# Kernel tuning notes

Measured on AMD Instinct MI355X. Metric: run time of the kernel, lower is better.

Reference implementation:

```python
import jax, jax.numpy as jnp
import numpy as np

WH, WW = 12, 12          # window height/width
N = WH * WW              # tokens per window (144)
HEADS = 16
DIM = 1024
C = DIM // 2             # attention channel dim (512)
HEAD_DIM = C // HEADS    # 32


def _rel_pos_index(wh, ww):
    ch, cw = np.arange(wh), np.arange(ww)
    coords = np.stack(np.meshgrid(ch, cw, indexing='ij')).reshape(2, -1)  # [2, N]
    rel = (coords[:, :, None] - coords[:, None, :]).transpose(1, 2, 0)    # [N, N, 2]
    rel = rel.copy()
    rel[:, :, 0] += wh - 1
    rel[:, :, 1] += ww - 1
    rel[:, :, 0] *= 2 * ww - 1
    return rel.sum(-1)  # [N, N] int


def _layernorm(x, g, b, eps=1e-5):
    mu = jnp.mean(x, axis=-1, keepdims=True)
    var = jnp.mean(jnp.square(x - mu), axis=-1, keepdims=True)
    return (x - mu) * jax.lax.rsqrt(var + eps) * g + b


def setup_inputs():
    key = jax.random.key(0)
    ks = jax.random.split(key, 10)
    std = 0.02
    inp = {
        'x': jax.random.normal(ks[0], (256, N, DIM), jnp.float32),
        'template': jax.random.normal(ks[1], (64, N, DIM), jnp.float32),
        'mask0': jnp.zeros((16, N, N), jnp.float32),
        'mask1': jnp.zeros((4, N, N), jnp.float32),
        's_H': 48, 's_W': 48, 't_H': 24, 't_W': 24,
        'rpb_table': jax.random.normal(ks[2], ((2 * WH - 1) * (2 * WW - 1), HEADS), jnp.float32) * std,
        'w_ps': jax.random.normal(ks[3], (DIM, C), jnp.float32) * std,
        'b_ps': jnp.zeros((C,), jnp.float32),
        'g_ps': jnp.ones((C,), jnp.float32),
        'be_ps': jnp.zeros((C,), jnp.float32),
        'w_pt': jax.random.normal(ks[4], (DIM, C), jnp.float32) * std,
        'b_pt': jnp.zeros((C,), jnp.float32),
        'g_pt': jnp.ones((C,), jnp.float32),
        'be_pt': jnp.zeros((C,), jnp.float32),
        'w_qkv': jax.random.normal(ks[5], (C, 3 * C), jnp.float32) * std,
        'b_qkv': jnp.zeros((3 * C,), jnp.float32),
        'w_tr': jax.random.normal(ks[6], (C, DIM), jnp.float32) * std,
        'b_tr': jnp.zeros((DIM,), jnp.float32),
        'w_sr': jax.random.normal(ks[7], (C, DIM), jnp.float32) * std,
        'b_sr': jnp.zeros((DIM,), jnp.float32),
    }
    return inp


def reference(x, template, mask0, mask1, s_H, s_W, t_H, t_W,
              rpb_table, w_ps, b_ps, g_ps, be_ps, w_pt, b_pt, g_pt, be_pt,
              w_qkv, b_qkv, w_tr, b_tr, w_sr, b_sr):
    scale = HEAD_DIM ** (-0.5)
    search_attn = _layernorm(x @ w_ps + b_ps, g_ps, be_ps)          # [Sw, N, C]
    template_attn = _layernorm(template @ w_pt + b_pt, g_pt, be_pt)  # [Tw, N, C]
    Sw, Tw = search_attn.shape[0], template_attn.shape[0]
    xa = jnp.concatenate([template_attn, search_attn], axis=0)      # [B_, N, C]
    B_, n, c = xa.shape

    qkv = (xa @ w_qkv + b_qkv).reshape(B_, n, 3, HEADS, HEAD_DIM)
    q = qkv[:, :, 0].transpose(0, 2, 1, 3) * scale  # [B_, H, N, Dh]
    k = qkv[:, :, 1].transpose(0, 2, 1, 3)
    v = qkv[:, :, 2].transpose(0, 2, 1, 3)

    idx = _rel_pos_index(WH, WW)  # numpy constant [N, N]
    bias = rpb_table[idx.reshape(-1)].reshape(n, n, HEADS).transpose(2, 0, 1)  # [H, N, N]

    attn = jnp.einsum('bhnd,bhmd->bhnm', q, k) + bias[None]  # [B_, H, N, N]

    attn_t, attn_s = attn[:Tw], attn[Tw:]
    nWs = mask0.shape[0]
    attn_s = (attn_s.reshape(Sw // nWs, nWs, HEADS, n, n) + mask0[None, :, None]).reshape(Sw, HEADS, n, n)
    nWt = mask1.shape[0]
    attn_t = (attn_t.reshape(Tw // nWt, nWt, HEADS, n, n) + mask1[None, :, None]).reshape(Tw, HEADS, n, n)
    attn = jax.nn.softmax(jnp.concatenate([attn_t, attn_s], axis=0), axis=-1)

    out = jnp.einsum('bhnm,bhmd->bhnd', attn, v).transpose(0, 2, 1, 3).reshape(B_, n, c)
    template_out = out[:Tw] @ w_tr + b_tr  # [Tw, N, DIM]
    search_out = out[Tw:] @ w_sr + b_sr    # [Sw, N, DIM]
    return (template_out, search_out)
```

## Files before the change

kernel.cpp:

```cpp
#include <hip/hip_runtime.h>


using s16x8 = __attribute__((ext_vector_type(8))) short;
using f32x4 = __attribute__((ext_vector_type(4))) float;
typedef __attribute__((ext_vector_type(2))) unsigned u32x2;

#define NTOK 144
#define NHEADS 16
#define CDIM 512
#define TROWS 9216
#define SROWS 36864
#define TOTROWS 46080
#define NWIN 320
#define NCLS 20

__device__ __forceinline__ unsigned short f2bf(float f) {
  unsigned u = __float_as_uint(f);
  u += 0x7fffu + ((u >> 16) & 1u);
  return (unsigned short)(u >> 16);
}
__device__ __forceinline__ float bf2f(unsigned short u) {
  return __uint_as_float(((unsigned)u) << 16);
}
__device__ __forceinline__ s16x8 mk8(unsigned a, unsigned b, unsigned c, unsigned d) {
  union { unsigned u[4]; s16x8 v; } x;
  x.u[0] = a; x.u[1] = b; x.u[2] = c; x.u[3] = d;
  return x.v;
}

__device__ __forceinline__ void gld16(const unsigned short* g, short* l) {
  __builtin_amdgcn_global_load_lds(
      (const __attribute__((address_space(1))) unsigned int*)g,
      (__attribute__((address_space(3))) unsigned int*)l, 16, 0, 0);
}


__global__ void transpose_cast(const float* __restrict__ w,
                               unsigned short* __restrict__ wT, int Kd, int Nd) {
  int i = blockIdx.x * 256 + threadIdx.x;
  if (i >= Kd * Nd) return;
  int n = i / Kd, k = i % Kd;
  wT[i] = f2bf(w[(size_t)k * Nd + n]);
}

__global__ __launch_bounds__(256) void cast_bf16(const float* __restrict__ in,
                                                 unsigned short* __restrict__ out, int n8) {
  int i = blockIdx.x * 256 + threadIdx.x;
  if (i >= n8) return;
  const float4* p = (const float4*)in + (size_t)i * 2;
  float4 f0 = p[0], f1 = p[1];
  s16x8 o;
  o[0] = (short)f2bf(f0.x); o[1] = (short)f2bf(f0.y);
  o[2] = (short)f2bf(f0.z); o[3] = (short)f2bf(f0.w);
  o[4] = (short)f2bf(f1.x); o[5] = (short)f2bf(f1.y);
  o[6] = (short)f2bf(f1.z); o[7] = (short)f2bf(f1.w);
  *(s16x8*)&out[(size_t)i * 8] = o;
}

__global__ void build_cmb(const float* __restrict__ rpb, const float* __restrict__ m0,
                          const float* __restrict__ m1, unsigned short* __restrict__ cmb) {
  int i = blockIdx.x * 256 + threadIdx.x;
  if (i >= NCLS * NHEADS * NTOK * NTOK) return;
  int cls = i / (NHEADS * NTOK * NTOK);
  int rem = i % (NHEADS * NTOK * NTOK);
  int h = rem / (NTOK * NTOK);
  int ij = rem % (NTOK * NTOK);
  int qi = ij / NTOK, kj = ij % NTOK;
  int dh = qi / 12 - kj / 12 + 11;
  int dw = qi % 12 - kj % 12 + 11;
  float bias = rpb[(dh * 23 + dw) * NHEADS + h];
  float mv = (cls < 4) ? m1[(size_t)cls * NTOK * NTOK + ij]
                       : m0[(size_t)(cls - 4) * NTOK * NTOK + ij];
  cmb[i] = f2bf(bias + mv);
}

template<int EPI>
__global__ __launch_bounds__(256) void gemm_glds(
    const unsigned short* __restrict__ Ab,
    const unsigned short* __restrict__ BTt, const unsigned short* __restrict__ BTs,
    const float* __restrict__ biast, const float* __restrict__ biass,
    void* __restrict__ Cout, int M, int N, int K)
{
  __shared__ short As[128 * 64];
  __shared__ short Bs[128 * 64];
  const int t = threadIdx.x;
  const int lane = t & 63, wv = t >> 6, lg = lane >> 4, lc = lane & 15;
  const int bn = blockIdx.x * 128, bm = blockIdx.y * 128;
  const bool isT = bm < TROWS;
  const unsigned short* BT = isT ? BTt : BTs;
  const float* bias = isT ? biast : biass;

  const int srow = 32 * wv + (lane >> 3);
  const int scol = (((lane & 7) ^ ((lane >> 3) & 7))) * 8;
  const unsigned short* aSrc = Ab + (size_t)(bm + srow) * K + scol;
  const unsigned short* bSrc = BT + (size_t)(bn + srow) * K + scol;
  const size_t rowK8 = (size_t)8 * K;

  f32x4 acc[2][8] = {};

  for (int kt = 0; kt < K; kt += 64) {
    __syncthreads();
#pragma unroll
    for (int i = 0; i < 4; i++) {
      gld16(aSrc + kt + i * rowK8, &As[(wv * 4 + i) * 512]);
      gld16(bSrc + kt + i * rowK8, &Bs[(wv * 4 + i) * 512]);
    }
    __syncthreads();
#pragma unroll
    for (int kk = 0; kk < 2; kk++) {
      const int csw = 8 * ((4 * kk + lg) ^ (lc & 7));
      const int r0 = wv * 32 + lc, r1 = r0 + 16;
      s16x8 a0 = *(const s16x8*)&As[r0 * 64 + csw];
      s16x8 a1 = *(const s16x8*)&As[r1 * 64 + csw];
#pragma unroll
      for (int nt = 0; nt < 8; nt++) {
        s16x8 bfr = *(const s16x8*)&Bs[(nt * 16 + lc) * 64 + csw];
        acc[0][nt] = __builtin_amdgcn_mfma_f32_16x16x32_bf16(a0, bfr, acc[0][nt], 0, 0, 0);
        acc[1][nt] = __builtin_amdgcn_mfma_f32_16x16x32_bf16(a1, bfr, acc[1][nt], 0, 0, 0);
      }
    }
  }

#pragma unroll
  for (int mt = 0; mt < 2; mt++) {
    const int rbase = bm + wv * 32 + mt * 16 + lg * 4;
#pragma unroll
    for (int nt = 0; nt < 8; nt++) {
      const int cg = bn + nt * 16 + lc;
#pragma unroll
      for (int r = 0; r < 4; r++) {
        const int rg = rbase + r;
        float val = acc[mt][nt][r] + bias[cg];
        if (EPI == 2) {
          ((float*)Cout)[(size_t)rg * N + cg] = val;
        } else {
          if (EPI == 1 && cg < 512) val *= 0.17677669529663687f;
          ((unsigned short*)Cout)[(size_t)rg * N + cg] = f2bf(val);
        }
      }
    }
  }
}

__global__ __launch_bounds__(256) void ln_kernel(
    unsigned short* __restrict__ xa,
    const float* __restrict__ g_pt, const float* __restrict__ be_pt,
    const float* __restrict__ g_ps, const float* __restrict__ be_ps)
{
  const int row = blockIdx.x * 4 + (threadIdx.x >> 6);
  const int lane = threadIdx.x & 63;
  const bool isT = row < TROWS;
  const float* gg = isT ? g_pt : g_ps;
  const float* be = isT ? be_pt : be_ps;
  unsigned short* p = xa + (size_t)row * CDIM;
  const int c0 = lane * 8;

  s16x8 v8 = *(const s16x8*)&p[c0];
  float f[8];
  float s = 0.f, s2 = 0.f;
#pragma unroll
  for (int i = 0; i < 8; i++) {
    float xv = bf2f((unsigned short)v8[i]);
    f[i] = xv; s += xv; s2 += xv * xv;
  }
#pragma unroll
  for (int d = 1; d < 64; d <<= 1) { s += __shfl_xor(s, d); s2 += __shfl_xor(s2, d); }
  float mu = s * (1.f / CDIM);
  float var = s2 * (1.f / CDIM) - mu * mu;
  float rs = rsqrtf(var + 1e-5f);

  float4 g0 = *(const float4*)&gg[c0], g1 = *(const float4*)&gg[c0 + 4];
  float4 e0 = *(const float4*)&be[c0], e1 = *(const float4*)&be[c0 + 4];
  float gv[8] = {g0.x, g0.y, g0.z, g0.w, g1.x, g1.y, g1.z, g1.w};
  float ev[8] = {e0.x, e0.y, e0.z, e0.w, e1.x, e1.y, e1.z, e1.w};
  s16x8 o;
#pragma unroll
  for (int i = 0; i < 8; i++)
    o[i] = (short)f2bf((f[i] - mu) * rs * gv[i] + ev[i]);
  *(s16x8*)&p[c0] = o;
}

__global__ __launch_bounds__(576) void attn_kernel(
    const unsigned short* __restrict__ qkv, const unsigned short* __restrict__ cmb,
    unsigned short* __restrict__ outp)
{
  __shared__ short VT[32 * 168];
  const int w = blockIdx.x >> 4, h = blockIdx.x & 15;
  const int t = threadIdx.x;
  const unsigned short* qb = qkv + (size_t)w * NTOK * 1536;
  const int hq = h * 32;

  {
    const int n = t >> 2, d0 = (t & 3) * 8;
    s16x8 vv = *(const s16x8*)&qb[(size_t)n * 1536 + 1024 + hq + d0];
#pragma unroll
    for (int i = 0; i < 8; i++) VT[(d0 + i) * 168 + n] = vv[i];
  }
  if (t < 512) VT[(t >> 4) * 168 + 144 + (t & 15)] = 0;
  __syncthreads();

  const int lane = t & 63, wv = t >> 6, lg = lane >> 4, lc = lane & 15;
  const int q = wv * 16 + lc;
  const f32x4 zero = {0.f, 0.f, 0.f, 0.f};

  const s16x8 qf = *(const s16x8*)&qb[(size_t)q * 1536 + hq + lg * 8];

  const int cls = (w < 64) ? (w & 3) : 4 + ((w - 64) & 15);
  const unsigned short* cm =
      cmb + ((size_t)cls * NHEADS + h) * (NTOK * NTOK) + (size_t)q * NTOK;
  uint2 cmr[9];
#pragma unroll
  for (int nt = 0; nt < 9; nt++)
    cmr[nt] = *(const uint2*)&cm[nt * 16 + lg * 4];

  f32x4 accS[9];
#pragma unroll
  for (int nt = 0; nt < 9; nt++) {
    s16x8 kf = *(const s16x8*)&qb[(size_t)(nt * 16 + lc) * 1536 + 512 + hq + lg * 8];
    accS[nt] = __builtin_amdgcn_mfma_f32_16x16x32_bf16(kf, qf, zero, 0, 0, 0);
  }

  float mx = -1e30f;
#pragma unroll
  for (int nt = 0; nt < 9; nt++) {
    accS[nt][0] += bf2f((unsigned short)(cmr[nt].x & 0xffff));
    accS[nt][1] += bf2f((unsigned short)(cmr[nt].x >> 16));
    accS[nt][2] += bf2f((unsigned short)(cmr[nt].y & 0xffff));
    accS[nt][3] += bf2f((unsigned short)(cmr[nt].y >> 16));
#pragma unroll
    for (int r = 0; r < 4; r++) mx = fmaxf(mx, accS[nt][r]);
  }
  mx = fmaxf(mx, __shfl_xor(mx, 16));
  mx = fmaxf(mx, __shfl_xor(mx, 32));

  float sum = 0.f;
#pragma unroll
  for (int nt = 0; nt < 9; nt++)
#pragma unroll
    for (int r = 0; r < 4; r++) {
      float e = __expf(accS[nt][r] - mx);
      accS[nt][r] = e;
      sum += e;
    }
  sum += __shfl_xor(sum, 16);
  sum += __shfl_xor(sum, 32);
  const float inv = 1.f / sum;

  unsigned pk0[9], pk1[9];
#pragma unroll
  for (int nt = 0; nt < 9; nt++) {
    pk0[nt] = (unsigned)f2bf(accS[nt][0]) | ((unsigned)f2bf(accS[nt][1]) << 16);
    pk1[nt] = (unsigned)f2bf(accS[nt][2]) | ((unsigned)f2bf(accS[nt][3]) << 16);
  }

#pragma unroll
  for (int dt = 0; dt < 2; dt++) {
    const short* vbase = &VT[(dt * 16 + lc) * 168];
    f32x4 accO = zero;
#pragma unroll
    for (int kk = 0; kk < 4; kk++) {
      u32x2 A0 = *(const u32x2*)&vbase[32 * kk + lg * 4];
      u32x2 A1 = *(const u32x2*)&vbase[32 * kk + 16 + lg * 4];
      s16x8 a = mk8(A0[0], A0[1], A1[0], A1[1]);
      s16x8 b = mk8(pk0[2 * kk], pk1[2 * kk], pk0[2 * kk + 1], pk1[2 * kk + 1]);
      accO = __builtin_amdgcn_mfma_f32_16x16x32_bf16(a, b, accO, 0, 0, 0);
    }
    {
      u32x2 A0 = *(const u32x2*)&vbase[128 + lg * 4];
      s16x8 a = mk8(A0[0], A0[1], 0u, 0u);
      s16x8 b = mk8(pk0[8], pk1[8], 0u, 0u);
      accO = __builtin_amdgcn_mfma_f32_16x16x32_bf16(a, b, accO, 0, 0, 0);
    }
    unsigned o0 = (unsigned)f2bf(accO[0] * inv) | ((unsigned)f2bf(accO[1] * inv) << 16);
    unsigned o1 = (unsigned)f2bf(accO[2] * inv) | ((unsigned)f2bf(accO[3] * inv) << 16);
    uint2 st; st.x = o0; st.y = o1;
    *(uint2*)&outp[(size_t)(w * NTOK + q) * CDIM + hq + dt * 16 + lg * 4] = st;
  }
}

extern "C" void kernel_launch(void* const* d_in, const int* in_sizes, int n_in,
                              void* d_out, int out_size, void* d_ws, size_t ws_size,
                              hipStream_t stream)
{
  const float* x     = (const float*)d_in[0];
  const float* tpl   = (const float*)d_in[1];
  const float* mask0 = (const float*)d_in[2];
  const float* mask1 = (const float*)d_in[3];
  const float* rpb   = (const float*)d_in[8];
  const float* w_ps  = (const float*)d_in[9];
  const float* b_ps  = (const float*)d_in[10];
  const float* g_ps  = (const float*)d_in[11];
  const float* be_ps = (const float*)d_in[12];
  const float* w_pt  = (const float*)d_in[13];
  const float* b_pt  = (const float*)d_in[14];
  const float* g_pt  = (const float*)d_in[15];
  const float* be_pt = (const float*)d_in[16];
  const float* w_qkv = (const float*)d_in[17];
  const float* b_qkv = (const float*)d_in[18];
  const float* w_tr  = (const float*)d_in[19];
  const float* b_tr  = (const float*)d_in[20];
  const float* w_sr  = (const float*)d_in[21];
  const float* b_sr  = (const float*)d_in[22];

  char* ws = (char*)d_ws;
  unsigned short* wpsT  = (unsigned short*)(ws + 0x0000000);
  unsigned short* wptT  = (unsigned short*)(ws + 0x0100000);
  unsigned short* wqkvT = (unsigned short*)(ws + 0x0200000);
  unsigned short* wtrT  = (unsigned short*)(ws + 0x0380000);
  unsigned short* wsrT  = (unsigned short*)(ws + 0x0480000);
  unsigned short* cmb   = (unsigned short*)(ws + 0x0580000);
  unsigned short* xa    = (unsigned short*)(ws + 0x1300000);
  unsigned short* Sa    = (unsigned short*)(ws + 0x4000000);
  unsigned short* qkvF  = (unsigned short*)(ws + 0x4000000);
  float* outb           = (float*)d_out;

  transpose_cast<<<2048, 256, 0, stream>>>(w_ps, wpsT, 1024, 512);
  transpose_cast<<<2048, 256, 0, stream>>>(w_pt, wptT, 1024, 512);
  transpose_cast<<<3072, 256, 0, stream>>>(w_qkv, wqkvT, 512, 1536);
  transpose_cast<<<2048, 256, 0, stream>>>(w_tr, wtrT, 512, 1024);
  transpose_cast<<<2048, 256, 0, stream>>>(w_sr, wsrT, 512, 1024);
  build_cmb<<<(NCLS * NHEADS * NTOK * NTOK + 255) / 256, 256, 0, stream>>>(rpb, mask0, mask1, cmb);

  cast_bf16<<<(TROWS * 1024 / 8 + 255) / 256, 256, 0, stream>>>(tpl, Sa, TROWS * 1024 / 8);
  cast_bf16<<<(SROWS * 1024 / 8 + 255) / 256, 256, 0, stream>>>(
      x, Sa + (size_t)TROWS * 1024, SROWS * 1024 / 8);

  gemm_glds<0><<<dim3(4, 360), 256, 0, stream>>>(Sa, wptT, wpsT, b_pt, b_ps,
                                                 xa, TOTROWS, CDIM, 1024);
  ln_kernel<<<TOTROWS / 4, 256, 0, stream>>>(xa, g_pt, be_pt, g_ps, be_ps);

  gemm_glds<1><<<dim3(12, 360), 256, 0, stream>>>(xa, wqkvT, wqkvT, b_qkv, b_qkv,
                                                  qkvF, TOTROWS, 1536, CDIM);
  attn_kernel<<<NWIN * NHEADS, 576, 0, stream>>>(qkvF, cmb, xa);

  gemm_glds<2><<<dim3(8, 360), 256, 0, stream>>>(xa, wtrT, wsrT, b_tr, b_sr,
                                                 outb, TOTROWS, 1024, CDIM);
}
```

Before: 505.5 us.

## Fuse fp32-to-bf16 input cast into first GEMM and double-buffer LDS tiles

```diff
diff --git a/kernel.cpp b/kernel.cpp
--- a/kernel.cpp
+++ b/kernel.cpp
@@ -41,20 +41,6 @@
   if (i >= Kd * Nd) return;
   int n = i / Kd, k = i % Kd;
   wT[i] = f2bf(w[(size_t)k * Nd + n]);
-}
-
-__global__ __launch_bounds__(256) void cast_bf16(const float* __restrict__ in,
-                                                 unsigned short* __restrict__ out, int n8) {
-  int i = blockIdx.x * 256 + threadIdx.x;
-  if (i >= n8) return;
-  const float4* p = (const float4*)in + (size_t)i * 2;
-  float4 f0 = p[0], f1 = p[1];
-  s16x8 o;
-  o[0] = (short)f2bf(f0.x); o[1] = (short)f2bf(f0.y);
-  o[2] = (short)f2bf(f0.z); o[3] = (short)f2bf(f0.w);
-  o[4] = (short)f2bf(f1.x); o[5] = (short)f2bf(f1.y);
-  o[6] = (short)f2bf(f1.z); o[7] = (short)f2bf(f1.w);
-  *(s16x8*)&out[(size_t)i * 8] = o;
 }
 
 __global__ void build_cmb(const float* __restrict__ rpb, const float* __restrict__ m0,
@@ -74,15 +60,15 @@
   cmb[i] = f2bf(bias + mv);
 }
 
-template<int EPI>
+template<int AF32, int EPI>
 __global__ __launch_bounds__(256) void gemm_glds(
-    const unsigned short* __restrict__ Ab,
+    const void* __restrict__ At, const void* __restrict__ Asrch,
     const unsigned short* __restrict__ BTt, const unsigned short* __restrict__ BTs,
     const float* __restrict__ biast, const float* __restrict__ biass,
     void* __restrict__ Cout, int M, int N, int K)
 {
-  __shared__ short As[128 * 64];
-  __shared__ short Bs[128 * 64];
+  __shared__ short As[2][128 * 64];
+  __shared__ short Bs[2][128 * 64];
   const int t = threadIdx.x;
   const int lane = t & 63, wv = t >> 6, lg = lane >> 4, lc = lane & 15;
   const int bn = blockIdx.x * 128, bm = blockIdx.y * 128;
@@ -91,35 +77,83 @@
   const float* bias = isT ? biast : biass;
 
   const int srow = 32 * wv + (lane >> 3);
-  const int scol = (((lane & 7) ^ ((lane >> 3) & 7))) * 8;
-  const unsigned short* aSrc = Ab + (size_t)(bm + srow) * K + scol;
+  const int scol = ((lane & 7) ^ ((lane >> 3) & 7)) * 8;
   const unsigned short* bSrc = BT + (size_t)(bn + srow) * K + scol;
   const size_t rowK8 = (size_t)8 * K;
 
+  const unsigned short* aB = nullptr;
+  const float* aFrow = nullptr;
+  if (AF32) {
+    const float* aF = (const float*)(isT ? At : Asrch) + (size_t)(isT ? bm : bm - TROWS) * K;
+    aFrow = aF + (size_t)(t >> 1) * K + (t & 1) * 32;
+  } else {
+    aB = (const unsigned short*)(isT ? At : Asrch) + (size_t)(isT ? bm : bm - TROWS) * K;
+  }
+  const unsigned short* aSrc = AF32 ? nullptr : aB + (size_t)srow * K + scol;
+
   f32x4 acc[2][8] = {};
-
-  for (int kt = 0; kt < K; kt += 64) {
-    __syncthreads();
+  float4 fr[8];
+
+  auto LOADA = [&](int kt) {
+#pragma unroll
+    for (int j = 0; j < 4; j++) {
+      fr[2 * j]     = *(const float4*)(aFrow + kt + j * 8);
+      fr[2 * j + 1] = *(const float4*)(aFrow + kt + j * 8 + 4);
+    }
+  };
+  auto STOREA = [&](int b) {
+    const int r = t >> 1;
+#pragma unroll
+    for (int j = 0; j < 4; j++) {
+      float4 f0 = fr[2 * j], f1 = fr[2 * j + 1];
+      s16x8 o;
+      o[0] = (short)f2bf(f0.x); o[1] = (short)f2bf(f0.y);
+      o[2] = (short)f2bf(f0.z); o[3] = (short)f2bf(f0.w);
+      o[4] = (short)f2bf(f1.x); o[5] = (short)f2bf(f1.y);
+      o[6] = (short)f2bf(f1.z); o[7] = (short)f2bf(f1.w);
+      const int g = (t & 1) * 4 + j;
+      const int p = g ^ (r & 7);
+      *(s16x8*)&As[b][r * 64 + p * 8] = o;
+    }
+  };
+  auto STAGE = [&](int b, int kt) {
 #pragma unroll
     for (int i = 0; i < 4; i++) {
-      gld16(aSrc + kt + i * rowK8, &As[(wv * 4 + i) * 512]);
-      gld16(bSrc + kt + i * rowK8, &Bs[(wv * 4 + i) * 512]);
-    }
-    __syncthreads();
+      if (!AF32) gld16(aSrc + kt + i * rowK8, &As[b][(wv * 4 + i) * 512]);
+      gld16(bSrc + kt + i * rowK8, &Bs[b][(wv * 4 + i) * 512]);
+    }
+  };
+  auto COMPUTE = [&](int b) {
 #pragma unroll
     for (int kk = 0; kk < 2; kk++) {
       const int csw = 8 * ((4 * kk + lg) ^ (lc & 7));
       const int r0 = wv * 32 + lc, r1 = r0 + 16;
-      s16x8 a0 = *(const s16x8*)&As[r0 * 64 + csw];
-      s16x8 a1 = *(const s16x8*)&As[r1 * 64 + csw];
+      s16x8 a0 = *(const s16x8*)&As[b][r0 * 64 + csw];
+      s16x8 a1 = *(const s16x8*)&As[b][r1 * 64 + csw];
 #pragma unroll
       for (int nt = 0; nt < 8; nt++) {
-        s16x8 bfr = *(const s16x8*)&Bs[(nt * 16 + lc) * 64 + csw];
+        s16x8 bfr = *(const s16x8*)&Bs[b][(nt * 16 + lc) * 64 + csw];
         acc[0][nt] = __builtin_amdgcn_mfma_f32_16x16x32_bf16(a0, bfr, acc[0][nt], 0, 0, 0);
         acc[1][nt] = __builtin_amdgcn_mfma_f32_16x16x32_bf16(a1, bfr, acc[1][nt], 0, 0, 0);
       }
     }
-  }
+  };
+
+  if (AF32) LOADA(0);
+  STAGE(0, 0);
+  if (AF32) STOREA(0);
+  __syncthreads();
+
+  int cur = 0;
+  for (int kt = 64; kt < K; kt += 64) {
+    if (AF32) LOADA(kt);
+    STAGE(cur ^ 1, kt);
+    COMPUTE(cur);
+    if (AF32) STOREA(cur ^ 1);
+    __syncthreads();
+    cur ^= 1;
+  }
+  COMPUTE(cur);
 
 #pragma unroll
   for (int mt = 0; mt < 2; mt++) {
@@ -310,7 +344,6 @@
   unsigned short* wsrT  = (unsigned short*)(ws + 0x0480000);
   unsigned short* cmb   = (unsigned short*)(ws + 0x0580000);
   unsigned short* xa    = (unsigned short*)(ws + 0x1300000);
-  unsigned short* Sa    = (unsigned short*)(ws + 0x4000000);
   unsigned short* qkvF  = (unsigned short*)(ws + 0x4000000);
   float* outb           = (float*)d_out;
 
@@ -321,18 +354,16 @@
   transpose_cast<<<2048, 256, 0, stream>>>(w_sr, wsrT, 512, 1024);
   build_cmb<<<(NCLS * NHEADS * NTOK * NTOK + 255) / 256, 256, 0, stream>>>(rpb, mask0, mask1, cmb);
 
-  cast_bf16<<<(TROWS * 1024 / 8 + 255) / 256, 256, 0, stream>>>(tpl, Sa, TROWS * 1024 / 8);
-  cast_bf16<<<(SROWS * 1024 / 8 + 255) / 256, 256, 0, stream>>>(
-      x, Sa + (size_t)TROWS * 1024, SROWS * 1024 / 8);
-
-  gemm_glds<0><<<dim3(4, 360), 256, 0, stream>>>(Sa, wptT, wpsT, b_pt, b_ps,
-                                                 xa, TOTROWS, CDIM, 1024);
+  gemm_glds<1, 0><<<dim3(4, 360), 256, 0, stream>>>(tpl, x, wptT, wpsT, b_pt, b_ps,
+                                                    xa, TOTROWS, CDIM, 1024);
   ln_kernel<<<TOTROWS / 4, 256, 0, stream>>>(xa, g_pt, be_pt, g_ps, be_ps);
 
-  gemm_glds<1><<<dim3(12, 360), 256, 0, stream>>>(xa, wqkvT, wqkvT, b_qkv, b_qkv,
-                                                  qkvF, TOTROWS, 1536, CDIM);
+  gemm_glds<0, 1><<<dim3(12, 360), 256, 0, stream>>>(
+      xa, xa + (size_t)TROWS * CDIM, wqkvT, wqkvT, b_qkv, b_qkv,
+      qkvF, TOTROWS, 1536, CDIM);
   attn_kernel<<<NWIN * NHEADS, 576, 0, stream>>>(qkvF, cmb, xa);
 
-  gemm_glds<2><<<dim3(8, 360), 256, 0, stream>>>(xa, wtrT, wsrT, b_tr, b_sr,
-                                                 outb, TOTROWS, 1024, CDIM);
-}
+  gemm_glds<0, 2><<<dim3(8, 360), 256, 0, stream>>>(
+      xa, xa + (size_t)TROWS * CDIM, wtrT, wsrT, b_tr, b_sr,
+      outb, TOTROWS, 1024, CDIM);
+}
```

Measured after the change: 541.1 us. 7.1% more time.
